# Kernel optimization log

Measured on AMD Instinct MI355X. Metric: run time of the kernel, lower is better.

## Reference

```python
import jax, jax.numpy as jnp
import numpy as np

DIM = 1024
NH = 8
HD = DIM // NH  # 128
E = 8
EPS = 1e-5


def rope_cos_sin(L, hd):
    # matches RotaryPositionEmbedding: emb = cat([freqs, freqs], -1)
    inv_freq = 1.0 / (10000.0 ** (jnp.arange(0, hd, 2, dtype=jnp.float32) / hd))
    freqs = jnp.arange(L, dtype=jnp.float32)[:, None] * inv_freq[None, :]  # (L, hd/2)
    emb = jnp.concatenate([freqs, freqs], axis=-1)  # (L, hd)
    return jnp.cos(emb), jnp.sin(emb)


def rotate_half(x):
    # interleaved rotate, as in the torch apply_rope
    x1 = x[..., 0::2]
    x2 = x[..., 1::2]
    return jnp.stack((-x2, x1), axis=-1).reshape(x.shape)


def rope(t, cos, sin):
    # t: (B,H,L,D); cos/sin: (L,D)
    return t * cos[None, None] + rotate_half(t) * sin[None, None]


def heads(t):
    B, L, C = t.shape
    return t.reshape(B, L, NH, HD).transpose(0, 2, 1, 3)  # (B,H,L,D)


def setup_inputs() -> dict:
    key = jax.random.key(0)
    ks = jax.random.split(key, 32)
    std = 0.02
    d = {}
    d['x'] = jax.random.normal(ks[0], (16, 512, DIM), jnp.float32)
    d['h_a'] = jax.random.normal(ks[1], (16, 256, DIM), jnp.float32)
    d['h_t'] = jax.random.normal(ks[2], (16, 256, DIM), jnp.float32)
    names = ['qa', 'ka', 'va', 'qt', 'kt', 'vt', 'o', 'ffn']
    for i, n in enumerate(names):
        d['W_' + n] = jax.random.normal(ks[3 + 2 * i], (E, DIM, DIM), jnp.float32) * std
        d['b_' + n] = jax.random.normal(ks[4 + 2 * i], (E, DIM), jnp.float32) * std
    d['gamma'] = jnp.ones((E, DIM), jnp.float32)
    d['beta'] = jnp.zeros((E, DIM), jnp.float32)
    d['gating_factor'] = jnp.zeros((E,), jnp.float32)
    d['expert_idx'] = 3
    return d


def reference(x, h_a, h_t,
              W_qa, b_qa, W_ka, b_ka, W_va, b_va,
              W_qt, b_qt, W_kt, b_kt, W_vt, b_vt,
              W_o, b_o, W_ffn, b_ffn,
              gamma, beta, gating_factor, expert_idx):
    e = expert_idx

    def lin(t, W, b):
        return t @ W[e].T + b[e]

    B, T, C = x.shape
    Ka = h_a.shape[1]
    Kt = h_t.shape[1]

    q_a = heads(lin(x, W_qa, b_qa))        # (B,H,T,D)
    q_t = heads(lin(x, W_qt, b_qt))
    k_a = heads(lin(h_a, W_ka, b_ka))      # (B,H,Ka,D)
    v_a = heads(lin(h_a, W_va, b_va))
    k_t = heads(lin(h_t, W_kt, b_kt))      # (B,H,Kt,D)
    v_t = heads(lin(h_t, W_vt, b_vt))

    cos_m, sin_m = rope_cos_sin(T, HD)
    q_a = rope(q_a, cos_m, sin_m)
    q_t = rope(q_t, cos_m, sin_m)
    cos_a, sin_a = rope_cos_sin(Ka, HD)
    k_a = rope(k_a, cos_a, sin_a)
    cos_t, sin_t = rope_cos_sin(Kt, HD)
    k_t = rope(k_t, cos_t, sin_t)

    ratio_g = jax.nn.sigmoid(gating_factor[e])
    s_a = jnp.einsum('bhtd,bhkd->bhtk', q_a, k_a)
    s_t = jnp.einsum('bhtd,bhkd->bhtk', q_t, k_t) * ratio_g
    scores = jnp.concatenate([s_a, s_t], axis=-1) / np.sqrt(HD)
    w = jax.nn.softmax(scores, axis=-1)            # (B,H,T,Ka+Kt)
    v = jnp.concatenate([v_a, v_t], axis=2)        # (B,H,Ka+Kt,D)
    out = jnp.einsum('bhtk,bhkd->bhtd', w, v)
    out = out.transpose(0, 2, 1, 3).reshape(B, T, C)
    out = lin(out, W_o, b_o)

    x = out + x
    # ffn: SmileMoENorm -> SmileMoELinear -> ReLU (no extra residual)
    mu = jnp.mean(x, axis=-1, keepdims=True)
    var = jnp.var(x, axis=-1, keepdims=True)
    xn = (x - mu) / jnp.sqrt(var + EPS) * gamma[e] + beta[e]
    x = jax.nn.relu(lin(xn, W_ffn, b_ffn))
    return x
```

## Files before the change

### kernel.cpp

```cpp
#include <hip/hip_runtime.h>
#include <stdint.h>

typedef __bf16 bf16x8 __attribute__((ext_vector_type(8)));
typedef float f32x4 __attribute__((ext_vector_type(4)));
typedef unsigned short u16x8 __attribute__((ext_vector_type(8)));

typedef const __attribute__((address_space(1))) void* gas_ptr;
typedef __attribute__((address_space(3))) void* las_ptr;
typedef const __attribute__((address_space(3))) char* lds_c3;

__device__ __forceinline__ void gload16(const void* g, void* l) {
  __builtin_amdgcn_global_load_lds((gas_ptr)g, (las_ptr)l, 16, 0, 0);
}

__device__ __forceinline__ bf16x8 dsread16(const char* p) {
  bf16x8 r;
  asm volatile("ds_read_b128 %0, %1" : "=v"(r) : "v"((lds_c3)p));
  return r;
}
__device__ __forceinline__ void dswrite2(char* p, uint32_t v) {
  asm volatile("ds_write_b16 %0, %1" : : "v"((las_ptr)p), "v"(v));
}
template <int OFF>
__device__ __forceinline__ float dswz(float x) {
  float r;
  asm volatile("ds_swizzle_b32 %0, %1 offset:%c2" : "=v"(r) : "v"(x), "i"(OFF));
  return r;
}

__device__ __forceinline__ unsigned short f2bf(float f) {
  uint32_t u = __float_as_uint(f);
  u += 0x7FFFu + ((u >> 16) & 1u);
  return (unsigned short)(u >> 16);
}

#define SB __builtin_amdgcn_sched_barrier(0)
#define BAR __builtin_amdgcn_s_barrier()
#define LGK0 asm volatile("s_waitcnt lgkmcnt(0)")

__device__ __forceinline__ void conv8(const float* __restrict__ src,
                                      unsigned short* __restrict__ dst, int i) {
  const float4* s4 = (const float4*)src;
  float4 a = s4[2 * i], b = s4[2 * i + 1];
  u16x8 r;
  r[0] = f2bf(a.x); r[1] = f2bf(a.y); r[2] = f2bf(a.z); r[3] = f2bf(a.w);
  r[4] = f2bf(b.x); r[5] = f2bf(b.y); r[6] = f2bf(b.z); r[7] = f2bf(b.w);
  *(u16x8*)&dst[(size_t)i * 8] = r;
}

__global__ __launch_bounds__(256)
void prep_all(const float* __restrict__ x, const float* __restrict__ h_a,
              const float* __restrict__ h_t,
              const float* W0, const float* W1, const float* W2, const float* W3,
              const float* W4, const float* W5, const float* W6, const float* W7,
              const int* __restrict__ eptr,
              unsigned short* __restrict__ XB, unsigned short* __restrict__ HAB,
              unsigned short* __restrict__ HTB, unsigned short* __restrict__ WW,
              float* __restrict__ cosb, float* __restrict__ sinb) {
  const int blk = blockIdx.x, tid = threadIdx.x;
  if (blk < 4096) {
    conv8(x, XB, blk * 256 + tid);
  } else if (blk < 6144) {
    conv8(h_a, HAB, (blk - 4096) * 256 + tid);
  } else if (blk < 8192) {
    conv8(h_t, HTB, (blk - 6144) * 256 + tid);
  } else if (blk < 12288) {
    const int w = (blk - 8192) >> 9;
    const int i = ((blk - 8192) & 511) * 256 + tid;
    const float* wp;
    switch (w) {
      case 0: wp = W0; break; case 1: wp = W1; break;
      case 2: wp = W2; break; case 3: wp = W3; break;
      case 4: wp = W4; break; case 5: wp = W5; break;
      case 6: wp = W6; break; default: wp = W7; break;
    }
    conv8(wp + (size_t)(*eptr) * 1048576, WW + (size_t)w * 1048576, i);
  } else {
    const int i = (blk - 12288) * 256 + tid;
    const int t = i >> 7, d = i & 127;
    const int f = d & 63;
    float invf = expf(-0.14391156831212787f * (float)f);
    float ang = (float)t * invf;
    float s, c;
    sincosf(ang, &s, &c);
    cosb[i] = c;
    sinb[i] = s;
  }
}

template <int MODE>
__global__ __launch_bounds__(512, 1)
void gemm3r(const unsigned short* __restrict__ A0, const unsigned short* __restrict__ A1,
            const unsigned short* __restrict__ A2,
            const unsigned short* __restrict__ W0, const unsigned short* __restrict__ W1,
            const unsigned short* __restrict__ W2, const unsigned short* __restrict__ W3,
            const unsigned short* __restrict__ W4, const unsigned short* __restrict__ W5,
            const float* __restrict__ bias0, const float* __restrict__ bias1,
            const float* __restrict__ bias2, const float* __restrict__ bias3,
            const float* __restrict__ bias4, const float* __restrict__ bias5,
            const int* __restrict__ eptr, const float* __restrict__ ctab,
            const float* __restrict__ stab,
            unsigned short* __restrict__ oQA, unsigned short* __restrict__ oQT,
            unsigned short* __restrict__ oKA, unsigned short* __restrict__ oKT,
            unsigned short* __restrict__ outV,
            const float* __restrict__ resid, float* __restrict__ outf) {
  __shared__ __align__(16) char AL[98304];
  __shared__ __align__(16) char BL[49152];
  const int tid = threadIdx.x;
  const int lane = tid & 63, wid = tid >> 6, fr = lane & 15, g = lane >> 4;
  const int wm = wid >> 1, wn = wid & 1;
  const int id = blockIdx.x;
  const int e = *eptr;

  const unsigned short* Asel;
  const unsigned short* Wsel;
  const float* bias;
  int bm, bn, z = 0, half = 0, cb0;
  bool isQ = true;
  if constexpr (MODE == 0) {
    const int swz = (id & 7) * 128 + (id >> 3);
    if (swz < 512) {
      bm = swz >> 4; bn = swz & 15;
    } else {
      isQ = false;
      const int s2 = swz - 512;
      z = s2 >> 8;
      bm = (s2 & 255) >> 4; bn = s2 & 15;
    }
    half = bn >> 3;
    cb0 = (bn & 7) * 128;
    Asel = isQ ? A0 : (z ? A2 : A1);
    Wsel = isQ ? (half ? W1 : W0) : (z ? (half ? W5 : W4) : (half ? W3 : W2));
    bias = (isQ ? (half ? bias1 : bias0)
                : (z ? (half ? bias5 : bias4) : (half ? bias3 : bias2))) + e * 1024;
  } else {
    const int swz = (id & 7) * 32 + (id >> 3);
    bm = swz >> 3; bn = swz & 7;
    cb0 = bn * 128;
    Asel = A0;
    Wsel = W0;
    bias = bias0 + e * 1024;
  }

  const char* Ab = (const char*)Asel + (size_t)bm * 256 * 2048;
  const char* Bb = (const char*)Wsel + (size_t)cb0 * 2048;

  const int csw = (((tid & 7) ^ ((tid >> 3) & 7)) << 4);
  const char* Ags = Ab + (tid >> 3) * 2048 + csw;
  const char* Bgs = Bb + (tid >> 3) * 2048 + csw;
  char* Ald = AL + tid * 16;
  char* Bld = BL + tid * 16;

#define STA(T, BUF)                                                         \
  { const char* s_ = Ags + (T) * 128;                                       \
    char* d_ = Ald + (BUF) * 32768;                                         \
    gload16(s_, d_);                  gload16(s_ + 131072, d_ + 8192);      \
    gload16(s_ + 262144, d_ + 16384); gload16(s_ + 393216, d_ + 24576); }
#define STB(T, BUF)                                                         \
  { const char* s_ = Bgs + (T) * 128;                                       \
    char* d_ = Bld + (BUF) * 16384;                                         \
    gload16(s_, d_);                  gload16(s_ + 131072, d_ + 8192); }

  const int lsw7 = fr & 7;
  const int ksel = (wid & 4) ? 4 : 0;
  const int cA = ((ksel + g) ^ lsw7) << 4;
  const int cB = (((4 - ksel) + g) ^ lsw7) << 4;
  const int arow = (wm * 64 + fr) * 128;
  const int brow = (wn * 64 + fr) * 128;

  f32x4 acc[4][4];
#pragma unroll
  for (int m = 0; m < 4; ++m)
#pragma unroll
    for (int n = 0; n < 4; ++n) acc[m][n] = f32x4{0.f, 0.f, 0.f, 0.f};
  bf16x8 af1[4], bf1[4], af2[4], bf2[4];

#define RDAB(BASEA, BASEB, C, AF, BF)                                       \
  { const char* pa_ = (BASEA) + arow + (C);                                 \
    const char* pb_ = (BASEB) + brow + (C);                                 \
    _Pragma("unroll") for (int m = 0; m < 4; ++m)                           \
        AF[m] = dsread16(pa_ + m * 2048);                                   \
    _Pragma("unroll") for (int n = 0; n < 4; ++n)                           \
        BF[n] = dsread16(pb_ + n * 2048); }

#define MF16(AF, BF)                                                        \
  __builtin_amdgcn_s_setprio(1);                                            \
  _Pragma("unroll") for (int m = 0; m < 4; ++m)                             \
    _Pragma("unroll") for (int n = 0; n < 4; ++n)                           \
        acc[m][n] = __builtin_amdgcn_mfma_f32_16x16x32_bf16(                \
            AF[m], BF[n], acc[m][n], 0, 0, 0);                              \
  __builtin_amdgcn_s_setprio(0);

  STA(0, 0); STB(0, 0); STA(1, 1); STB(1, 1);

  int bc = 0;
#pragma unroll 1
  for (int t = 0; t < 16; ++t) {
    SB;
    if (t <= 14) asm volatile("s_waitcnt vmcnt(6)");
    else         asm volatile("s_waitcnt vmcnt(0)");
    BAR; SB;
    const char* ALc = AL + bc * 32768;
    const char* BLc = BL + bc * 16384;
    const int bs = bc ? bc - 1 : 2;
    RDAB(ALc, BLc, cA, af1, bf1);
    RDAB(ALc, BLc, cB, af2, bf2);
    SB;
    if (t <= 13) { STA(t + 2, bs); STB(t + 2, bs); }
    SB;
    asm volatile("s_waitcnt lgkmcnt(8)");
    SB;
    MF16(af1, bf1) SB;
    LGK0; SB;
    MF16(af2, bf2) SB;
    bc = (bc == 2) ? 0 : bc + 1;
  }
#undef RDAB
#undef MF16
#undef STA
#undef STB

  const int wrow0 = bm * 256 + wm * 64;
#pragma unroll
  for (int m = 0; m < 4; ++m) {
#pragma unroll
    for (int n = 0; n < 4; ++n) {
      const int lc = wn * 64 + n * 16 + fr;
      const int gc = cb0 + lc;
      const float bv = bias[gc];
#pragma unroll
      for (int j = 0; j < 4; ++j) {
        const int grow = wrow0 + m * 16 + g * 4 + j;
        float v = acc[m][n][j] + bv;
        if constexpr (MODE == 0) {
          const int hh = gc >> 7, dd = gc & 127;
          if (isQ) {
            const int tt = grow & 511, bb = grow >> 9;
            float pv = __shfl_xor(v, 1);
            float cs = ctab[tt * 128 + dd], sn = stab[tt * 128 + dd];
            float rh = (dd & 1) ? pv : -pv;
            float o = v * cs + rh * sn;
            unsigned short* dst = half ? oQT : oQA;
            dst[(((size_t)(bb * 8 + hh) * 512 + tt) << 7) + dd] = f2bf(o);
          } else {
            const int tt = grow & 255, bb = grow >> 8;
            if (half == 0) {
              float pv = __shfl_xor(v, 1);
              float cs = ctab[tt * 128 + dd], sn = stab[tt * 128 + dd];
              float rh = (dd & 1) ? pv : -pv;
              float o = v * cs + rh * sn;
              unsigned short* dst = z ? oKT : oKA;
              dst[(((size_t)(bb * 8 + hh) * 256 + tt) << 7) + dd] = f2bf(o);
            } else {
              outV[(((size_t)(bb * 8 + hh) << 7) + dd) * 512 + z * 256 + tt] = f2bf(v);
            }
          }
        } else {
          const size_t idx = ((size_t)grow << 10) + gc;
          if constexpr (MODE == 2) outf[idx] = v + resid[idx];
          else outf[idx] = fmaxf(v, 0.f);
        }
      }
    }
  }
}

__global__ __launch_bounds__(256, 2)
void attn_kernel(const unsigned short* __restrict__ QA, const unsigned short* __restrict__ QT,
                 const unsigned short* __restrict__ KA, const unsigned short* __restrict__ KT,
                 const unsigned short* __restrict__ VT,
                 unsigned short* __restrict__ AO,
                 const float* __restrict__ gating, const int* __restrict__ eptr) {
  __shared__ unsigned short Ks[2][8192];
  __shared__ unsigned short Vs[2][8192];
  __shared__ unsigned short Ps[8192];
  const int tid = threadIdx.x, lane = tid & 63, wv = tid >> 6;
  const int fr = lane & 15, g = lane >> 4;
  const int bid = blockIdx.x;
  const int b = bid >> 5, h = (bid >> 2) & 7, q0 = (bid & 3) << 7;
  const float ratio = 1.f / (1.f + __expf(-gating[*eptr]));
  const float SC = 0.08838834764831845f;
  const size_t bh = (size_t)(b * 8 + h);

  bf16x8 qf[2][4];
  {
    const char* qa = (const char*)QA + ((bh * 512 + q0 + wv * 32 + fr) << 8) + g * 16;
#pragma unroll
    for (int mb = 0; mb < 2; ++mb)
#pragma unroll
      for (int kb = 0; kb < 4; ++kb)
        qf[mb][kb] = *(const bf16x8*)(qa + mb * 4096 + kb * 64);
  }

  auto stage = [&](int t, int buf) {
    const char* kgb = (const char*)((t < 4) ? KA : KT) + ((bh * 256 + ((size_t)(t & 3) << 6)) << 8);
    const char* vgb = (const char*)VT + (bh << 17) + (t << 7);
    char* ksd = (char*)Ks[buf] + tid * 16;
    char* vsd = (char*)Vs[buf] + tid * 16;
#pragma unroll
    for (int j = 0; j < 4; ++j) {
      const int rk = j * 16 + (tid >> 4);
      const int ck = ((tid & 15) << 4) ^ ((rk & 7) << 4);
      gload16(kgb + rk * 256 + ck, ksd + j * 4096);
      const int dv = j * 32 + (tid >> 3);
      const int cv = ((tid & 7) << 4) ^ ((dv & 7) << 4);
      gload16(vgb + dv * 1024 + cv, vsd + j * 4096);
    }
  };

  float m_run[2][4], l_run[2][4];
  f32x4 oacc[2][8];
#pragma unroll
  for (int mb = 0; mb < 2; ++mb) {
#pragma unroll
    for (int j = 0; j < 4; ++j) { m_run[mb][j] = -1e30f; l_run[mb][j] = 0.f; }
#pragma unroll
    for (int db = 0; db < 8; ++db) oacc[mb][db] = f32x4{0.f, 0.f, 0.f, 0.f};
  }

  stage(0, 0);

  for (int it = 0; it < 8; ++it) {
    const int cur = it & 1;
    if (it < 7) stage(it + 1, cur ^ 1);
    SB;
    if (it < 7) asm volatile("s_waitcnt vmcnt(8)");
    else        asm volatile("s_waitcnt vmcnt(0)");
    SB;
    BAR;
    SB;

    if (it == 4) {
      const char* qt = (const char*)QT + ((bh * 512 + q0 + wv * 32 + fr) << 8) + g * 16;
#pragma unroll
      for (int mb = 0; mb < 2; ++mb)
#pragma unroll
        for (int kb = 0; kb < 4; ++kb)
          qf[mb][kb] = *(const bf16x8*)(qt + mb * 4096 + kb * 64);
    }
    const float sc = (it < 4) ? SC : SC * ratio;
    const char* kc = (const char*)Ks[cur];
    const char* vc = (const char*)Vs[cur];

    f32x4 s[2][4];
#pragma unroll
    for (int mb = 0; mb < 2; ++mb)
#pragma unroll
      for (int nb = 0; nb < 4; ++nb) s[mb][nb] = f32x4{0.f, 0.f, 0.f, 0.f};
    bf16x8 kfa[4], kfb[4];
#pragma unroll
    for (int kb = 0; kb < 4; ++kb) {
      const int byt = (fr * 256 + kb * 64 + g * 16) ^ ((fr & 7) << 4);
      kfa[kb] = dsread16(kc + byt);
    }
#pragma unroll
    for (int nb = 0; nb < 4; ++nb) {
      if (nb < 3) {
#pragma unroll
        for (int kb = 0; kb < 4; ++kb) {
          const int r = (nb + 1) * 16 + fr;
          const int byt = (r * 256 + kb * 64 + g * 16) ^ ((r & 7) << 4);
          if (nb & 1) kfa[kb] = dsread16(kc + byt);
          else        kfb[kb] = dsread16(kc + byt);
        }
        asm volatile("s_waitcnt lgkmcnt(4)");
      } else {
        asm volatile("s_waitcnt lgkmcnt(0)");
      }
      SB;
      __builtin_amdgcn_s_setprio(1);
#pragma unroll
      for (int kb = 0; kb < 4; ++kb) {
        bf16x8 kf = (nb & 1) ? kfb[kb] : kfa[kb];
        s[0][nb] = __builtin_amdgcn_mfma_f32_16x16x32_bf16(qf[0][kb], kf, s[0][nb], 0, 0, 0);
        s[1][nb] = __builtin_amdgcn_mfma_f32_16x16x32_bf16(qf[1][kb], kf, s[1][nb], 0, 0, 0);
      }
      __builtin_amdgcn_s_setprio(0);
    }
    SB;

    float red[8];
#pragma unroll
    for (int mb = 0; mb < 2; ++mb)
#pragma unroll
      for (int j = 0; j < 4; ++j) {
        float mx = -1e30f;
#pragma unroll
        for (int nb = 0; nb < 4; ++nb) {
          s[mb][nb][j] *= sc;
          mx = fmaxf(mx, s[mb][nb][j]);
        }
        red[mb * 4 + j] = mx;
      }
#define MAXR(OFF)                                                        \
    { float tmp[8];                                                      \
      _Pragma("unroll") for (int k = 0; k < 8; ++k) tmp[k] = dswz<OFF>(red[k]); \
      asm volatile("s_waitcnt lgkmcnt(0)");                              \
      SB;                                                                \
      _Pragma("unroll") for (int k = 0; k < 8; ++k) red[k] = fmaxf(red[k], tmp[k]); }
    MAXR(0x041F) MAXR(0x081F) MAXR(0x101F) MAXR(0x201F)
#undef MAXR
#pragma unroll
    for (int mb = 0; mb < 2; ++mb)
#pragma unroll
      for (int j = 0; j < 4; ++j) {
        const float mn = fmaxf(m_run[mb][j], red[mb * 4 + j]);
        const float alpha = __expf(m_run[mb][j] - mn);
        m_run[mb][j] = mn;
        l_run[mb][j] *= alpha;
#pragma unroll
        for (int db = 0; db < 8; ++db) oacc[mb][db][j] *= alpha;
      }
#pragma unroll
    for (int mb = 0; mb < 2; ++mb)
#pragma unroll
      for (int nb = 0; nb < 4; ++nb)
#pragma unroll
        for (int j = 0; j < 4; ++j) {
          float p = __expf(s[mb][nb][j] - m_run[mb][j]);
          l_run[mb][j] += p;
          const int r = wv * 32 + mb * 16 + g * 4 + j;
          const int byt = (r * 128 + (nb * 16 + fr) * 2) ^ ((r & 7) << 4);
          dswrite2((char*)Ps + byt, (uint32_t)f2bf(p));
        }

#pragma unroll
    for (int kb2 = 0; kb2 < 2; ++kb2) {
      bf16x8 pf[2], vf[8];
#pragma unroll
      for (int mb = 0; mb < 2; ++mb) {
        const int r = wv * 32 + mb * 16 + fr;
        const int byt = (r * 128 + kb2 * 64 + g * 16) ^ ((r & 7) << 4);
        pf[mb] = dsread16((const char*)Ps + byt);
      }
#pragma unroll
      for (int db = 0; db < 8; ++db) {
        const int rv = db * 16 + fr;
        const int byt = (rv * 128 + kb2 * 64 + g * 16) ^ ((rv & 7) << 4);
        vf[db] = dsread16(vc + byt);
      }
      asm volatile("s_waitcnt lgkmcnt(0)");
      SB;
      __builtin_amdgcn_s_setprio(1);
#pragma unroll
      for (int db = 0; db < 8; ++db) {
        oacc[0][db] = __builtin_amdgcn_mfma_f32_16x16x32_bf16(pf[0], vf[db], oacc[0][db], 0, 0, 0);
        oacc[1][db] = __builtin_amdgcn_mfma_f32_16x16x32_bf16(pf[1], vf[db], oacc[1][db], 0, 0, 0);
      }
      __builtin_amdgcn_s_setprio(0);
    }
    SB;
    BAR;
  }

#pragma unroll
  for (int mb = 0; mb < 2; ++mb)
#pragma unroll
    for (int j = 0; j < 4; ++j) {
      float lt = l_run[mb][j];
#pragma unroll
      for (int d = 1; d < 16; d <<= 1) lt += __shfl_xor(lt, d);
      float inv = 1.f / lt;
#pragma unroll
      for (int db = 0; db < 8; ++db) {
        float o = oacc[mb][db][j] * inv;
        int row = q0 + wv * 32 + mb * 16 + g * 4 + j;
        int col = h * 128 + db * 16 + fr;
        AO[(((size_t)b * 512 + row) << 10) + col] = f2bf(o);
      }
    }
}

__global__ __launch_bounds__(256)
void ln_kernel(const float* __restrict__ X2, const float* __restrict__ gbase,
               const float* __restrict__ bbase, const int* __restrict__ eptr,
               unsigned short* __restrict__ XN) {
  const int row = blockIdx.x, tid = threadIdx.x;
  const float* x = X2 + ((size_t)row << 10);
  float4 v = ((const float4*)x)[tid];
  float s = v.x + v.y + v.z + v.w;
  float ss = v.x * v.x + v.y * v.y + v.z * v.z + v.w * v.w;
#pragma unroll
  for (int d = 1; d < 64; d <<= 1) {
    s += __shfl_xor(s, d);
    ss += __shfl_xor(ss, d);
  }
  __shared__ float red[8];
  const int wv = tid >> 6, lane = tid & 63;
  if (lane == 0) { red[wv] = s; red[4 + wv] = ss; }
  __syncthreads();
  s = red[0] + red[1] + red[2] + red[3];
  ss = red[4] + red[5] + red[6] + red[7];
  const float mu = s * 0.0009765625f;
  const float var = ss * 0.0009765625f - mu * mu;
  const float inv = rsqrtf(var + 1e-5f);
  const int e = *eptr;
  const float* gg = gbase + e * 1024 + tid * 4;
  const float* bb = bbase + e * 1024 + tid * 4;
  ushort4 o;
  o.x = f2bf((v.x - mu) * inv * gg[0] + bb[0]);
  o.y = f2bf((v.y - mu) * inv * gg[1] + bb[1]);
  o.z = f2bf((v.z - mu) * inv * gg[2] + bb[2]);
  o.w = f2bf((v.w - mu) * inv * gg[3] + bb[3]);
  *(ushort4*)&XN[((size_t)row << 10) + tid * 4] = o;
}

extern "C" void kernel_launch(void* const* d_in, const int* in_sizes, int n_in,
                              void* d_out, int out_size, void* d_ws, size_t ws_size,
                              hipStream_t stream) {
  (void)in_sizes; (void)n_in; (void)out_size; (void)ws_size;
  const float* x      = (const float*)d_in[0];
  const float* h_a    = (const float*)d_in[1];
  const float* h_t    = (const float*)d_in[2];
  const float* W_qa   = (const float*)d_in[3];
  const float* b_qa   = (const float*)d_in[4];
  const float* W_ka   = (const float*)d_in[5];
  const float* b_ka   = (const float*)d_in[6];
  const float* W_va   = (const float*)d_in[7];
  const float* b_va   = (const float*)d_in[8];
  const float* W_qt   = (const float*)d_in[9];
  const float* b_qt   = (const float*)d_in[10];
  const float* W_kt   = (const float*)d_in[11];
  const float* b_kt   = (const float*)d_in[12];
  const float* W_vt   = (const float*)d_in[13];
  const float* b_vt   = (const float*)d_in[14];
  const float* W_o    = (const float*)d_in[15];
  const float* b_o    = (const float*)d_in[16];
  const float* W_ffn  = (const float*)d_in[17];
  const float* b_ffn  = (const float*)d_in[18];
  const float* gamma  = (const float*)d_in[19];
  const float* beta   = (const float*)d_in[20];
  const float* gating = (const float*)d_in[21];
  const int*   eptr   = (const int*)d_in[22];

  char* ws = (char*)d_ws;
  unsigned short* XB  = (unsigned short*)(ws + 0);
  unsigned short* HAB = (unsigned short*)(ws + 16777216);
  unsigned short* HTB = (unsigned short*)(ws + 25165824);
  float*          X2  = (float*)(ws + 0);
  unsigned short* WW  = (unsigned short*)(ws + 33554432);
  unsigned short* QAb = (unsigned short*)(ws + 50331648);
  unsigned short* XN  = QAb;
  unsigned short* QTb = (unsigned short*)(ws + 67108864);
  unsigned short* KAb = (unsigned short*)(ws + 83886080);
  unsigned short* KTb = (unsigned short*)(ws + 92274688);
  unsigned short* VTb = (unsigned short*)(ws + 100663296);
  unsigned short* AOb = (unsigned short*)(ws + 117440512);
  float* COS = (float*)(ws + 134217728);
  float* SIN = (float*)(ws + 134479872);

  prep_all<<<12544, 256, 0, stream>>>(x, h_a, h_t,
      W_qa, W_ka, W_va, W_qt, W_kt, W_vt, W_o, W_ffn, eptr,
      XB, HAB, HTB, WW, COS, SIN);

  gemm3r<0><<<dim3(1024), 512, 0, stream>>>(XB, HAB, HTB,
      WW + 0ull * 1048576, WW + 3ull * 1048576,
      WW + 1ull * 1048576, WW + 2ull * 1048576,
      WW + 4ull * 1048576, WW + 5ull * 1048576,
      b_qa, b_qt, b_ka, b_va, b_kt, b_vt,
      eptr, COS, SIN,
      QAb, QTb, KAb, KTb, VTb, nullptr, nullptr);

  attn_kernel<<<512, 256, 0, stream>>>(QAb, QTb, KAb, KTb, VTb, AOb, gating, eptr);

  gemm3r<2><<<dim3(256), 512, 0, stream>>>(AOb, nullptr, nullptr,
      WW + 6ull * 1048576, nullptr, nullptr, nullptr, nullptr, nullptr,
      b_o, nullptr, nullptr, nullptr, nullptr, nullptr,
      eptr, nullptr, nullptr,
      nullptr, nullptr, nullptr, nullptr, nullptr, x, X2);

  ln_kernel<<<8192, 256, 0, stream>>>(X2, gamma, beta, eptr, XN);

  gemm3r<3><<<dim3(256), 512, 0, stream>>>(XN, nullptr, nullptr,
      WW + 7ull * 1048576, nullptr, nullptr, nullptr, nullptr, nullptr,
      b_ffn, nullptr, nullptr, nullptr, nullptr, nullptr,
      eptr, nullptr, nullptr,
      nullptr, nullptr, nullptr, nullptr, nullptr, nullptr, (float*)d_out);
}
```

Baseline: 259.3 us.

## Store residual sum as bf16, split GEMM k-loop reads, swizzle attention blocks

The W_o GEMM epilogue now writes the residual sum x+out as bf16 instead of fp32, and the layernorm kernel reads bf16. This halves the intermediate write and read traffic but loses precision before layernorm. The GEMM main loop now reads one half-tile of fragments, issues half of the next-stage loads and runs MFMAs, then repeats for the second half. This cuts fragment registers at the cost of a full lgkm wait before each MFMA batch. Attention blocks are remapped with an XCD-style swizzle to improve cache locality.

```diff
diff --git a/kernel.cpp b/kernel.cpp
--- a/kernel.cpp
+++ b/kernel.cpp
@@ -32,6 +32,9 @@
   uint32_t u = __float_as_uint(f);
   u += 0x7FFFu + ((u >> 16) & 1u);
   return (unsigned short)(u >> 16);
+}
+__device__ __forceinline__ float bf2f(unsigned short u) {
+  return __uint_as_float(((uint32_t)u) << 16);
 }
 
 #define SB __builtin_amdgcn_sched_barrier(0)
@@ -103,7 +106,8 @@
             unsigned short* __restrict__ oQA, unsigned short* __restrict__ oQT,
             unsigned short* __restrict__ oKA, unsigned short* __restrict__ oKT,
             unsigned short* __restrict__ outV,
-            const float* __restrict__ resid, float* __restrict__ outf) {
+            const float* __restrict__ resid, unsigned short* __restrict__ outbf,
+            float* __restrict__ outf) {
   __shared__ __align__(16) char AL[98304];
   __shared__ __align__(16) char BL[49152];
   const int tid = threadIdx.x;
@@ -173,22 +177,22 @@
   for (int m = 0; m < 4; ++m)
 #pragma unroll
     for (int n = 0; n < 4; ++n) acc[m][n] = f32x4{0.f, 0.f, 0.f, 0.f};
-  bf16x8 af1[4], bf1[4], af2[4], bf2[4];
-
-#define RDAB(BASEA, BASEB, C, AF, BF)                                       \
+  bf16x8 af[4], bf[4];
+
+#define RDAB(BASEA, BASEB, C)                                               \
   { const char* pa_ = (BASEA) + arow + (C);                                 \
     const char* pb_ = (BASEB) + brow + (C);                                 \
     _Pragma("unroll") for (int m = 0; m < 4; ++m)                           \
-        AF[m] = dsread16(pa_ + m * 2048);                                   \
+        af[m] = dsread16(pa_ + m * 2048);                                   \
     _Pragma("unroll") for (int n = 0; n < 4; ++n)                           \
-        BF[n] = dsread16(pb_ + n * 2048); }
-
-#define MF16(AF, BF)                                                        \
+        bf[n] = dsread16(pb_ + n * 2048); }
+
+#define MF16                                                                \
   __builtin_amdgcn_s_setprio(1);                                            \
   _Pragma("unroll") for (int m = 0; m < 4; ++m)                             \
     _Pragma("unroll") for (int n = 0; n < 4; ++n)                           \
         acc[m][n] = __builtin_amdgcn_mfma_f32_16x16x32_bf16(                \
-            AF[m], BF[n], acc[m][n], 0, 0, 0);                              \
+            af[m], bf[n], acc[m][n], 0, 0, 0);                              \
   __builtin_amdgcn_s_setprio(0);
 
   STA(0, 0); STB(0, 0); STA(1, 1); STB(1, 1);
@@ -203,16 +207,14 @@
     const char* ALc = AL + bc * 32768;
     const char* BLc = BL + bc * 16384;
     const int bs = bc ? bc - 1 : 2;
-    RDAB(ALc, BLc, cA, af1, bf1);
-    RDAB(ALc, BLc, cB, af2, bf2);
-    SB;
-    if (t <= 13) { STA(t + 2, bs); STB(t + 2, bs); }
-    SB;
-    asm volatile("s_waitcnt lgkmcnt(8)");
-    SB;
-    MF16(af1, bf1) SB;
-    LGK0; SB;
-    MF16(af2, bf2) SB;
+    RDAB(ALc, BLc, cA); SB;
+    if (t <= 13) STA(t + 2, bs);
+    SB; LGK0; SB;
+    MF16 SB;
+    RDAB(ALc, BLc, cB); SB;
+    if (t <= 13) STB(t + 2, bs);
+    SB; LGK0; SB;
+    MF16 SB;
     bc = (bc == 2) ? 0 : bc + 1;
   }
 #undef RDAB
@@ -255,10 +257,12 @@
               outV[(((size_t)(bb * 8 + hh) << 7) + dd) * 512 + z * 256 + tt] = f2bf(v);
             }
           }
+        } else if constexpr (MODE == 2) {
+          const size_t idx = ((size_t)grow << 10) + gc;
+          outbf[idx] = f2bf(v + resid[idx]);
         } else {
           const size_t idx = ((size_t)grow << 10) + gc;
-          if constexpr (MODE == 2) outf[idx] = v + resid[idx];
-          else outf[idx] = fmaxf(v, 0.f);
+          outf[idx] = fmaxf(v, 0.f);
         }
       }
     }
@@ -276,7 +280,8 @@
   __shared__ unsigned short Ps[8192];
   const int tid = threadIdx.x, lane = tid & 63, wv = tid >> 6;
   const int fr = lane & 15, g = lane >> 4;
-  const int bid = blockIdx.x;
+  const int id = blockIdx.x;
+  const int bid = (id & 7) * 64 + (id >> 3);
   const int b = bid >> 5, h = (bid >> 2) & 7, q0 = (bid & 3) << 7;
   const float ratio = 1.f / (1.f + __expf(-gating[*eptr]));
   const float SC = 0.08838834764831845f;
@@ -472,14 +477,15 @@
 }
 
 __global__ __launch_bounds__(256)
-void ln_kernel(const float* __restrict__ X2, const float* __restrict__ gbase,
+void ln_kernel(const unsigned short* __restrict__ X2, const float* __restrict__ gbase,
                const float* __restrict__ bbase, const int* __restrict__ eptr,
                unsigned short* __restrict__ XN) {
   const int row = blockIdx.x, tid = threadIdx.x;
-  const float* x = X2 + ((size_t)row << 10);
-  float4 v = ((const float4*)x)[tid];
-  float s = v.x + v.y + v.z + v.w;
-  float ss = v.x * v.x + v.y * v.y + v.z * v.z + v.w * v.w;
+  const unsigned short* x = X2 + ((size_t)row << 10);
+  ushort4 raw = ((const ushort4*)x)[tid];
+  float v0 = bf2f(raw.x), v1 = bf2f(raw.y), v2 = bf2f(raw.z), v3 = bf2f(raw.w);
+  float s = v0 + v1 + v2 + v3;
+  float ss = v0 * v0 + v1 * v1 + v2 * v2 + v3 * v3;
 #pragma unroll
   for (int d = 1; d < 64; d <<= 1) {
     s += __shfl_xor(s, d);
@@ -498,10 +504,10 @@
   const float* gg = gbase + e * 1024 + tid * 4;
   const float* bb = bbase + e * 1024 + tid * 4;
   ushort4 o;
-  o.x = f2bf((v.x - mu) * inv * gg[0] + bb[0]);
-  o.y = f2bf((v.y - mu) * inv * gg[1] + bb[1]);
-  o.z = f2bf((v.z - mu) * inv * gg[2] + bb[2]);
-  o.w = f2bf((v.w - mu) * inv * gg[3] + bb[3]);
+  o.x = f2bf((v0 - mu) * inv * gg[0] + bb[0]);
+  o.y = f2bf((v1 - mu) * inv * gg[1] + bb[1]);
+  o.z = f2bf((v2 - mu) * inv * gg[2] + bb[2]);
+  o.w = f2bf((v3 - mu) * inv * gg[3] + bb[3]);
   *(ushort4*)&XN[((size_t)row << 10) + tid * 4] = o;
 }
 
@@ -537,7 +543,7 @@
   unsigned short* XB  = (unsigned short*)(ws + 0);
   unsigned short* HAB = (unsigned short*)(ws + 16777216);
   unsigned short* HTB = (unsigned short*)(ws + 25165824);
-  float*          X2  = (float*)(ws + 0);
+  unsigned short* X2b = (unsigned short*)(ws + 0);
   unsigned short* WW  = (unsigned short*)(ws + 33554432);
   unsigned short* QAb = (unsigned short*)(ws + 50331648);
   unsigned short* XN  = QAb;
@@ -559,7 +565,7 @@
       WW + 4ull * 1048576, WW + 5ull * 1048576,
       b_qa, b_qt, b_ka, b_va, b_kt, b_vt,
       eptr, COS, SIN,
-      QAb, QTb, KAb, KTb, VTb, nullptr, nullptr);
+      QAb, QTb, KAb, KTb, VTb, nullptr, nullptr, nullptr);
 
   attn_kernel<<<512, 256, 0, stream>>>(QAb, QTb, KAb, KTb, VTb, AOb, gating, eptr);
 
@@ -567,13 +573,13 @@
       WW + 6ull * 1048576, nullptr, nullptr, nullptr, nullptr, nullptr,
       b_o, nullptr, nullptr, nullptr, nullptr, nullptr,
       eptr, nullptr, nullptr,
-      nullptr, nullptr, nullptr, nullptr, nullptr, x, X2);
-
-  ln_kernel<<<8192, 256, 0, stream>>>(X2, gamma, beta, eptr, XN);
+      nullptr, nullptr, nullptr, nullptr, nullptr, x, X2b, nullptr);
+
+  ln_kernel<<<8192, 256, 0, stream>>>(X2b, gamma, beta, eptr, XN);
 
   gemm3r<3><<<dim3(256), 512, 0, stream>>>(XN, nullptr, nullptr,
       WW + 7ull * 1048576, nullptr, nullptr, nullptr, nullptr, nullptr,
       b_ffn, nullptr, nullptr, nullptr, nullptr, nullptr,
       eptr, nullptr, nullptr,
-      nullptr, nullptr, nullptr, nullptr, nullptr, nullptr, (float*)d_out);
-}
+      nullptr, nullptr, nullptr, nullptr, nullptr, nullptr, nullptr, (float*)d_out);
+}
```

After: 247.0 us. 1.05x faster.
